# Performance work log

Hardware: AMD Instinct MI355X
Metric: run time of the kernel (lower is better)

The kernel has to match this reference:

```python
import jax, jax.numpy as jnp
import numpy as np

V, E, H, L, C, NH, O, B = 32000, 128, 128, 6, 4, 4, 1024, 16384
HD = H // NH


def setup_inputs() -> dict:
    key = jax.random.key(0)
    ks = jax.random.split(key, 20)
    s = 1.0 / np.sqrt(H).astype(np.float32)

    def rn(k, shape, scale=s):
        return jax.random.normal(k, shape, jnp.float32) * scale

    return {
        "tokens": jax.random.randint(ks[0], (B, 1), 0, V),
        "h": jax.random.normal(ks[1], (L, C, B, H), jnp.float32),
        "emb": rn(ks[2], (V, E), 1.0),
        "wih0_c0": rn(ks[3], (3 * H, E)),
        "wih0_rest": rn(ks[4], (C - 1, 3 * H, 1)),
        "bih0": rn(ks[5], (C, 3 * H)),
        "whh0": rn(ks[6], (C, 3 * H, H)),
        "bhh0": rn(ks[7], (C, 3 * H)),
        "wih": rn(ks[8], (L - 1, C, 3 * H, H)),
        "whh": rn(ks[9], (L - 1, C, 3 * H, H)),
        "bih": rn(ks[10], (L - 1, C, 3 * H)),
        "bhh": rn(ks[11], (L - 1, C, 3 * H)),
        "attn_in_w": rn(ks[12], (L, 3 * H, H)),
        "attn_in_b": rn(ks[13], (L, 3 * H)),
        "attn_out_w": rn(ks[14], (L, H, H), 0.001),  # nn.init.normal_(out_proj.weight, 0, 0.001)
        "attn_out_b": jnp.zeros((L, H), jnp.float32),
        "ln_g": jnp.ones((L, H), jnp.float32),
        "ln_b": jnp.zeros((L, H), jnp.float32),
        "gate_w": rn(ks[15], (L, 2 * H)),
        "gate_b": jnp.zeros((L,), jnp.float32),
        "head_w": rn(ks[16], (O, H)),
        "head_b": jnp.zeros((O,), jnp.float32),
    }


def _gru(gi, gh, h):
    # torch GRUCell: r,z gates sigmoid; n = tanh(in + r*hn); h' = (1-z)*n + z*h
    ir, iz, i_n = jnp.split(gi, 3, -1)
    hr, hz, h_n = jnp.split(gh, 3, -1)
    r = jax.nn.sigmoid(ir + hr)
    z = jax.nn.sigmoid(iz + hz)
    n = jnp.tanh(i_n + r * h_n)
    return (1.0 - z) * n + z * h


def _msg_layer(hn, in_w, in_b, out_w, out_b, g, b):
    # hn: [C,B,H]; MultiheadAttention with batch_first=False (seq=C), then LayerNorm
    qkv = jnp.einsum('cbh,gh->cbg', hn, in_w) + in_b
    q, k, v = jnp.split(qkv, 3, -1)
    q = q.reshape(C, -1, NH, HD)
    k = k.reshape(C, -1, NH, HD)
    v = v.reshape(C, -1, NH, HD)
    scores = jnp.einsum('qbnd,kbnd->bnqk', q, k) / np.sqrt(HD).astype(np.float32)
    a = jax.nn.softmax(scores, axis=-1)
    o = jnp.einsum('bnqk,kbnd->qbnd', a, v).reshape(C, -1, H)
    o = jnp.einsum('cbh,oh->cbo', o, out_w) + out_b
    mu = o.mean(-1, keepdims=True)
    var = o.var(-1, keepdims=True)
    return (o - mu) / jnp.sqrt(var + 1e-5) * g + b


def reference(tokens, h, emb, wih0_c0, wih0_rest, bih0, whh0, bhh0, wih, whh, bih, bhh,
              attn_in_w, attn_in_b, attn_out_w, attn_out_b, ln_g, ln_b,
              gate_w, gate_b, head_w, head_b):
    bsz = tokens.shape[0]
    x0 = emb[tokens[:, 0]]  # [B,E]
    x = None
    h_new = []
    for l in range(L):
        hl = h[l]  # [C,B,H]
        if l == 0:
            gi0 = x0 @ wih0_c0.T + bih0[0]  # col 0 gets the embedding
            # cols 1..C-1 get a zeros(B,1) dummy input -> x @ wih0_rest == 0, bias only
            gi_rest = jnp.broadcast_to(bih0[1:, None, :], (C - 1, bsz, 3 * H))
            gi = jnp.concatenate([gi0[None], gi_rest], 0)
            whh_l, bhh_l = whh0, bhh0
        else:
            gi = jnp.einsum('cbi,cgi->cbg', x, wih[l - 1]) + bih[l - 1][:, None, :]
            whh_l, bhh_l = whh[l - 1], bhh[l - 1]
        gh = jnp.einsum('cbi,cgi->cbg', hl, whh_l) + bhh_l[:, None, :]
        hl_n = _gru(gi, gh, hl)
        msg = _msg_layer(hl_n, attn_in_w[l], attn_in_b[l], attn_out_w[l], attn_out_b[l], ln_g[l], ln_b[l])
        gin = jnp.concatenate([hl_n, msg], -1)  # [C,B,2H]
        gt = jax.nn.sigmoid(jnp.einsum('cbh,h->cb', gin, gate_w[l]) + gate_b[l])[..., None]
        hl_n = (1.0 - gt) * hl_n + gt * msg
        h_new.append(hl_n)
        x = hl_n
    h_n = jnp.stack(h_new, 0)  # [L,C,B,H]
    y = h_n[-1, 0] @ head_w.T + head_b  # head on last layer, column 0
    return (y, h_n)
```

## Files before the change

kernel.cpp:

```cpp
#include <hip/hip_runtime.h>
#include <hip/hip_bf16.h>

#define B_   16384
#define H_   128
#define C_   4
#define L_   6
#define O_   1024
#define G3H  384
#define CB   (C_ * B_)
#define CBH  (C_ * B_ * H_)

typedef __hip_bfloat16 bf16;
using bf16x8  = __attribute__((ext_vector_type(8))) __bf16;
using bf16x4  = __attribute__((ext_vector_type(4))) __bf16;
using floatx4 = __attribute__((ext_vector_type(4))) float;

__device__ __forceinline__ bf16 f2bf(float x) { return __float2bfloat16(x); }
__device__ __forceinline__ float bf2f(bf16 x) { return __bfloat162float(x); }
__device__ __forceinline__ void store_val(float* p, float v) { *p = v; }
__device__ __forceinline__ void store_val(bf16* p, float v) { *p = f2bf(v); }

__device__ __forceinline__ floatx4 mfma16(bf16x8 a, bf16x8 b, floatx4 c) {
  return __builtin_amdgcn_mfma_f32_16x16x32_bf16(a, b, c, 0, 0, 0);
}

__device__ __forceinline__ bf16x8 load8(const bf16* p) { return *(const bf16x8*)p; }
__device__ __forceinline__ bf16x8 load8(const float* p) {
  const float4 a = *(const float4*)p;
  const float4 b = *(const float4*)(p + 4);
  bf16x8 r;
  r[0] = (__bf16)a.x; r[1] = (__bf16)a.y; r[2] = (__bf16)a.z; r[3] = (__bf16)a.w;
  r[4] = (__bf16)b.x; r[5] = (__bf16)b.y; r[6] = (__bf16)b.z; r[7] = (__bf16)b.w;
  return r;
}

__device__ __forceinline__ float wave_sum(float x) {
#pragma unroll
  for (int off = 32; off; off >>= 1) x += __shfl_xor(x, off);
  return x;
}

__device__ __forceinline__ float sigmoidf_(float x) {
  return 1.f / (1.f + __expf(-x));
}
__device__ __forceinline__ float tanhf_(float x) {
  float e = __expf(2.f * x);
  return 1.f - 2.f / (e + 1.f);
}

struct Cvt7 {
  const float* src[7];
  long start4[8];
};
__global__ __launch_bounds__(256) void cvt7_kernel(Cvt7 a, bf16* __restrict__ dst) {
  long i4 = (long)blockIdx.x * 256 + threadIdx.x;
  if (i4 >= a.start4[7]) return;
  int s = 0;
#pragma unroll
  for (int k = 1; k < 7; ++k)
    if (i4 >= a.start4[k]) s = k;
  const float4 v = ((const float4*)a.src[s])[i4 - a.start4[s]];
  bf16x4 o;
  o[0] = (__bf16)v.x; o[1] = (__bf16)v.y; o[2] = (__bf16)v.z; o[3] = (__bf16)v.w;
  ((bf16x4*)dst)[i4] = o;
}

template <typename AT, typename OutT>
__global__ __launch_bounds__(256) void gemm_bt(const AT* __restrict__ A,
                                               const bf16* __restrict__ W,
                                               const float* __restrict__ bias,
                                               OutT* __restrict__ out,
                                               int N, int rows_per_batch,
                                               long wstride, long bstride) {
  const int wave = threadIdx.x >> 6;
  const int lane = threadIdx.x & 63;
  const int m0   = blockIdx.x * 16;
  const int n0   = blockIdx.y * 64 + wave * 16;
  const int sub  = lane & 15;
  const int quad = lane >> 4;
  const int batch = m0 / rows_per_batch;
  const bf16*  Wb = W + (long)batch * wstride;
  const float* Bi = bias + (long)batch * bstride;

  const AT*   Ap = A + (long)(m0 + sub) * 128 + quad * 8;
  const bf16* Wp = Wb + (long)(n0 + sub) * 128 + quad * 8;

  floatx4 acc = {0.f, 0.f, 0.f, 0.f};
#pragma unroll
  for (int kc = 0; kc < 4; ++kc) {
    acc = mfma16(load8(Ap + kc * 32), load8(Wp + kc * 32), acc);
  }

  const int col = n0 + sub;
  const float bv = Bi[col];
#pragma unroll
  for (int r = 0; r < 4; ++r) {
    long row = m0 + quad * 4 + r;
    store_val(&out[row * (long)N + col], acc[r] + bv);
  }
}

__global__ __launch_bounds__(128) void embed_kernel(const int* __restrict__ tok,
                                                    const float* __restrict__ emb,
                                                    bf16* __restrict__ x0) {
  const int b = blockIdx.x;
  x0[(long)b * 128 + threadIdx.x] = f2bf(emb[(long)tok[b] * 128 + threadIdx.x]);
}

template <bool L0>
__global__ __launch_bounds__(256) void cell_fused(const float* __restrict__ x,
                                                  const bf16* __restrict__ x0,
                                                  const bf16* __restrict__ wih_l,
                                                  const float* __restrict__ bih_l,
                                                  const float* __restrict__ h,
                                                  const bf16* __restrict__ whh_l,
                                                  const float* __restrict__ bhh_l,
                                                  const bf16* __restrict__ ainw,
                                                  const float* __restrict__ ainb,
                                                  float* __restrict__ hn,
                                                  bf16* __restrict__ qkv) {
  __shared__ __align__(16) char lds[3 * 16384];
  char* h_raw  = lds;
  char* x_raw  = lds + 16384;
  char* hn_raw = lds + 32768;

  const int tid = threadIdx.x;
  const int wave = tid >> 6, lane = tid & 63;
  const int sub = lane & 15, quad = lane >> 4;
  const int m0 = blockIdx.x * 64;
  const int cell = m0 / B_;
  const bool has_gi = (!L0) || (cell == 0);

  {
    const int colg = tid & 15;
    const int rb   = tid >> 4;
#pragma unroll
    for (int i = 0; i < 4; ++i) {
      const int row = i * 16 + rb;
      bf16x8 v = load8(h + (long)(m0 + row) * H_ + colg * 8);
      const int boff = (row * 256 + colg * 16) ^ ((row & 7) << 4);
      *(bf16x8*)(h_raw + boff) = v;
    }
    if (has_gi) {
      if constexpr (L0) {
#pragma unroll
        for (int i = 0; i < 4; ++i) {
          const int row = i * 16 + rb;
          bf16x8 v = load8(x0 + (long)(m0 + row) * H_ + colg * 8);
          const int boff = (row * 256 + colg * 16) ^ ((row & 7) << 4);
          *(bf16x8*)(x_raw + boff) = v;
        }
      } else {
#pragma unroll
        for (int i = 0; i < 4; ++i) {
          const int row = i * 16 + rb;
          bf16x8 v = load8(x + (long)(m0 + row) * H_ + colg * 8);
          const int boff = (row * 256 + colg * 16) ^ ((row & 7) << 4);
          *(bf16x8*)(x_raw + boff) = v;
        }
      }
    }
  }
  __syncthreads();

  const bf16*  Wh = whh_l + (long)cell * G3H * H_;
  const bf16*  Wi = L0 ? wih_l : wih_l + (long)cell * G3H * H_;
  const float* bh = bhh_l + cell * G3H;
  const float* bi = bih_l + cell * G3H;

#pragma unroll
  for (int p = 0; p < 2; ++p) {
    const int colr = wave * 32 + p * 16 + sub;

    bf16x8 wfr[3][4], wif[3][4];
#pragma unroll
    for (int g = 0; g < 3; ++g) {
      const bf16* Wg = Wh + (long)(g * 128 + colr) * H_ + quad * 8;
#pragma unroll
      for (int kc = 0; kc < 4; ++kc) wfr[g][kc] = load8(Wg + kc * 32);
    }
    if (has_gi) {
#pragma unroll
      for (int g = 0; g < 3; ++g) {
        const bf16* Wg = Wi + (long)(g * 128 + colr) * H_ + quad * 8;
#pragma unroll
        for (int kc = 0; kc < 4; ++kc) wif[g][kc] = load8(Wg + kc * 32);
      }
    }

    const float bir = bi[colr],        bhr = bh[colr];
    const float biz = bi[128 + colr],  bhz = bh[128 + colr];
    const float bin_ = bi[256 + colr], bhn = bh[256 + colr];

#pragma unroll
    for (int rt = 0; rt < 4; ++rt) {
      bf16x8 hfr[4];
#pragma unroll
      for (int kc = 0; kc < 4; ++kc) {
        const int lrow = rt * 16 + sub;
        const int boff = (lrow * 256 + kc * 64 + quad * 16) ^ ((lrow & 7) << 4);
        hfr[kc] = *(const bf16x8*)(h_raw + boff);
      }
      floatx4 ar = {0.f, 0.f, 0.f, 0.f}, az = {0.f, 0.f, 0.f, 0.f};
      floatx4 anh = {0.f, 0.f, 0.f, 0.f}, ani = {0.f, 0.f, 0.f, 0.f};
#pragma unroll
      for (int kc = 0; kc < 4; ++kc) {
        ar  = mfma16(hfr[kc], wfr[0][kc], ar);
        az  = mfma16(hfr[kc], wfr[1][kc], az);
        anh = mfma16(hfr[kc], wfr[2][kc], anh);
      }
      if (has_gi) {
        bf16x8 xfr[4];
#pragma unroll
        for (int kc = 0; kc < 4; ++kc) {
          const int lrow = rt * 16 + sub;
          const int boff = (lrow * 256 + kc * 64 + quad * 16) ^ ((lrow & 7) << 4);
          xfr[kc] = *(const bf16x8*)(x_raw + boff);
        }
#pragma unroll
        for (int kc = 0; kc < 4; ++kc) {
          ar  = mfma16(xfr[kc], wif[0][kc], ar);
          az  = mfma16(xfr[kc], wif[1][kc], az);
          ani = mfma16(xfr[kc], wif[2][kc], ani);
        }
      }

#pragma unroll
      for (int r = 0; r < 4; ++r) {
        const int lrow = rt * 16 + quad * 4 + r;
        const long grow = m0 + lrow;
        float rg = sigmoidf_(ar[r] + bir + bhr);
        float zg = sigmoidf_(az[r] + biz + bhz);
        float ng = tanhf_(ani[r] + bin_ + rg * (anh[r] + bhn));
        float hv = h[grow * H_ + colr];
        float hnv = (1.f - zg) * ng + zg * hv;
        hn[grow * H_ + colr] = hnv;
        const int boff = (lrow * 256 + colr * 2) ^ ((lrow & 7) << 4);
        *(bf16*)(hn_raw + boff) = f2bf(hnv);
      }
    }
  }
  __syncthreads();

#pragma unroll
  for (int t = 0; t < 6; ++t) {
    const int col = wave * 96 + t * 16 + sub;
    bf16x8 wf[4];
    const bf16* Wp = ainw + (long)col * H_ + quad * 8;
#pragma unroll
    for (int kc = 0; kc < 4; ++kc) wf[kc] = load8(Wp + kc * 32);
    const float bv = ainb[col];
#pragma unroll
    for (int rp = 0; rp < 2; ++rp) {
      bf16x8 af0[4], af1[4];
#pragma unroll
      for (int kc = 0; kc < 4; ++kc) {
        const int lr0 = (2 * rp) * 16 + sub, lr1 = (2 * rp + 1) * 16 + sub;
        af0[kc] = *(const bf16x8*)(hn_raw +
                   ((lr0 * 256 + kc * 64 + quad * 16) ^ ((lr0 & 7) << 4)));
        af1[kc] = *(const bf16x8*)(hn_raw +
                   ((lr1 * 256 + kc * 64 + quad * 16) ^ ((lr1 & 7) << 4)));
      }
      floatx4 acc0 = {0.f, 0.f, 0.f, 0.f}, acc1 = {0.f, 0.f, 0.f, 0.f};
#pragma unroll
      for (int kc = 0; kc < 4; ++kc) {
        acc0 = mfma16(af0[kc], wf[kc], acc0);
        acc1 = mfma16(af1[kc], wf[kc], acc1);
      }
#pragma unroll
      for (int r = 0; r < 4; ++r) {
        qkv[(long)(m0 + (2 * rp) * 16 + quad * 4 + r) * G3H + col] = f2bf(acc0[r] + bv);
        qkv[(long)(m0 + (2 * rp + 1) * 16 + quad * 4 + r) * G3H + col] = f2bf(acc1[r] + bv);
      }
    }
  }
}

__global__ __launch_bounds__(256) void attn_oproj(const bf16* __restrict__ qkv,
                                                  const bf16* __restrict__ w,
                                                  const float* __restrict__ bias,
                                                  const float* __restrict__ g,
                                                  const float* __restrict__ bb,
                                                  const float* __restrict__ gatew,
                                                  const float* __restrict__ gateb,
                                                  float* __restrict__ hn) {
  __shared__ __align__(16) char lds[49152 + 16384];
  bf16*  qkv_s = (bf16*)lds;
  float* o2_s  = (float*)lds;
  char*  o_raw = lds + 49152;

  const int tid = threadIdx.x;
  const int b0 = blockIdx.x * 16;

#pragma unroll
  for (int i = 0; i < 12; ++i) {
    const int idx = i * 256 + tid;
    const int r = idx / 48, ch = idx - r * 48;
    const int c = r >> 4, bj = r & 15;
    bf16x8 v = load8(qkv + ((long)c * B_ + b0 + bj) * G3H + ch * 8);
    *(bf16x8*)(qkv_s + r * 384 + ch * 8) = v;
  }
  __syncthreads();

  {
    const int d = tid & 31;
    const int pair = tid >> 5;
#pragma unroll
    for (int pi = 0; pi < 8; ++pi) {
      const int idx = pi * 8 + pair;
      const int bj = idx >> 2, head = idx & 3;
      float q[C_], k[C_], v[C_];
#pragma unroll
      for (int c = 0; c < C_; ++c) {
        const bf16* row = qkv_s + (c * 16 + bj) * 384 + head * 32 + d;
        q[c] = bf2f(row[0]);
        k[c] = bf2f(row[128]);
        v[c] = bf2f(row[256]);
      }
      float a[C_][C_];
#pragma unroll
      for (int qc = 0; qc < C_; ++qc) {
#pragma unroll
        for (int kc = 0; kc < C_; ++kc) {
          float pdot = q[qc] * k[kc];
#pragma unroll
          for (int off = 16; off; off >>= 1) pdot += __shfl_xor(pdot, off, 32);
          a[qc][kc] = pdot * 0.17677669529663687f;
        }
      }
#pragma unroll
      for (int qc = 0; qc < C_; ++qc) {
        float m = fmaxf(fmaxf(a[qc][0], a[qc][1]), fmaxf(a[qc][2], a[qc][3]));
        float s = 0.f;
#pragma unroll
        for (int kc = 0; kc < C_; ++kc) {
          a[qc][kc] = __expf(a[qc][kc] - m);
          s += a[qc][kc];
        }
        float inv = 1.f / s;
        float ov = 0.f;
#pragma unroll
        for (int kc = 0; kc < C_; ++kc) ov += a[qc][kc] * v[kc];
        const int orow = qc * 16 + bj;
        const int boff = (orow * 256 + (head * 32 + d) * 2) ^ ((orow & 7) << 4);
        *(bf16*)(o_raw + boff) = f2bf(ov * inv);
      }
    }
  }
  __syncthreads();

  {
    const int wave = tid >> 6, lane = tid & 63;
    const int sub = lane & 15, quad = lane >> 4;
#pragma unroll
    for (int p = 0; p < 2; ++p) {
      const int col = wave * 32 + p * 16 + sub;
      bf16x8 wf[4];
      const bf16* Wp = w + (long)col * H_ + quad * 8;
#pragma unroll
      for (int kc = 0; kc < 4; ++kc) wf[kc] = load8(Wp + kc * 32);
      const float bv = bias[col];
#pragma unroll
      for (int rt = 0; rt < 4; ++rt) {
        bf16x8 af[4];
#pragma unroll
        for (int kc = 0; kc < 4; ++kc) {
          const int lrow = rt * 16 + sub;
          af[kc] = *(const bf16x8*)(o_raw +
                    ((lrow * 256 + kc * 64 + quad * 16) ^ ((lrow & 7) << 4)));
        }
        floatx4 acc = {0.f, 0.f, 0.f, 0.f};
#pragma unroll
        for (int kc = 0; kc < 4; ++kc) acc = mfma16(af[kc], wf[kc], acc);
#pragma unroll
        for (int r = 0; r < 4; ++r)
          o2_s[(rt * 16 + quad * 4 + r) * 132 + col] = acc[r] + bv;
      }
    }
  }
  __syncthreads();

  {
    const int wave = tid >> 6, lane = tid & 63;
#pragma unroll
    for (int rr = 0; rr < 16; ++rr) {
      const int row = wave * 16 + rr;
      const int j1 = lane, j2 = lane + 64;
      float v1 = o2_s[row * 132 + j1], v2 = o2_s[row * 132 + j2];
      float mu = wave_sum(v1 + v2) * (1.f / 128.f);
      float d1 = v1 - mu, d2 = v2 - mu;
      float var = wave_sum(d1 * d1 + d2 * d2) * (1.f / 128.f);
      float rs = rsqrtf(var + 1e-5f);
      float m1 = d1 * rs * g[j1] + bb[j1];
      float m2 = d2 * rs * g[j2] + bb[j2];
      const int qc = row >> 4, bj = row & 15;
      const long grow = (long)qc * B_ + b0 + bj;
      float h1 = hn[grow * H_ + j1], h2 = hn[grow * H_ + j2];
      float gp = h1 * gatew[j1] + m1 * gatew[128 + j1] +
                 h2 * gatew[j2] + m2 * gatew[128 + j2];
      float gt = 1.f / (1.f + __expf(-(wave_sum(gp) + gateb[0])));
      hn[grow * H_ + j1] = (1.f - gt) * h1 + gt * m1;
      hn[grow * H_ + j2] = (1.f - gt) * h2 + gt * m2;
    }
  }
}

extern "C" void kernel_launch(void* const* d_in, const int* in_sizes, int n_in,
                              void* d_out, int out_size, void* d_ws, size_t ws_size,
                              hipStream_t stream) {
  const int*   tokens = (const int*)d_in[0];
  const float* h      = (const float*)d_in[1];
  const float* emb    = (const float*)d_in[2];
  const float* wih0c0 = (const float*)d_in[3];
  const float* bih0   = (const float*)d_in[5];
  const float* whh0   = (const float*)d_in[6];
  const float* bhh0   = (const float*)d_in[7];
  const float* wih    = (const float*)d_in[8];
  const float* whh    = (const float*)d_in[9];
  const float* bih    = (const float*)d_in[10];
  const float* bhh    = (const float*)d_in[11];
  const float* ainw   = (const float*)d_in[12];
  const float* ainb   = (const float*)d_in[13];
  const float* aoutw  = (const float*)d_in[14];
  const float* aoutb  = (const float*)d_in[15];
  const float* lng    = (const float*)d_in[16];
  const float* lnb    = (const float*)d_in[17];
  const float* gw     = (const float*)d_in[18];
  const float* gb     = (const float*)d_in[19];
  const float* headw  = (const float*)d_in[20];
  const float* headb  = (const float*)d_in[21];

  float* y_out  = (float*)d_out;
  float* hn_out = (float*)d_out + (long)B_ * O_;

  bf16* ws = (bf16*)d_ws;
  bf16* bufA = ws;
  bf16* x0   = bufA + (long)CB * G3H;
  bf16* wp   = x0 + (long)CB * H_;
  bf16* wih0bf  = wp;                  wp += 49152;
  bf16* whh0bf  = wp;                  wp += 196608;
  bf16* wihbf   = wp;                  wp += 983040;
  bf16* whhbf   = wp;                  wp += 983040;
  bf16* ainwbf  = wp;                  wp += 294912;
  bf16* aoutwbf = wp;                  wp += 98304;
  bf16* headwbf = wp;                  wp += 131072;

  dim3 blk(256);

  {
    Cvt7 a;
    const float* srcs[7] = {wih0c0, whh0, wih, whh, ainw, aoutw, headw};
    const long lens[7] = {49152, 196608, 983040, 983040, 294912, 98304, 131072};
    long cum = 0;
    for (int i = 0; i < 7; ++i) { a.src[i] = srcs[i]; a.start4[i] = cum / 4; cum += lens[i]; }
    a.start4[7] = cum / 4;
    const long n4 = cum / 4;
    cvt7_kernel<<<(int)((n4 + 255) / 256), blk, 0, stream>>>(a, wih0bf);
  }

  embed_kernel<<<B_, 128, 0, stream>>>(tokens, emb, x0);

  for (int l = 0; l < L_; ++l) {
    float* hn_l = hn_out + (long)l * CBH;
    const float* hl = h + (long)l * CBH;

    if (l == 0) {
      cell_fused<true><<<CB / 64, blk, 0, stream>>>(
          nullptr, x0, wih0bf, bih0, hl, whh0bf, bhh0,
          ainwbf, ainb, hn_l, bufA);
    } else {
      cell_fused<false><<<CB / 64, blk, 0, stream>>>(
          hn_out + (long)(l - 1) * CBH, nullptr,
          wihbf + (long)(l - 1) * C_ * G3H * H_, bih + (long)(l - 1) * C_ * G3H,
          hl, whhbf + (long)(l - 1) * C_ * G3H * H_, bhh + (long)(l - 1) * C_ * G3H,
          ainwbf + (long)l * G3H * H_, ainb + (long)l * G3H, hn_l, bufA);
    }

    attn_oproj<<<B_ / 16, blk, 0, stream>>>(
        bufA, aoutwbf + (long)l * H_ * H_, aoutb + (long)l * H_,
        lng + l * H_, lnb + l * H_, gw + l * 2 * H_, gb + l, hn_l);
  }

  gemm_bt<float, float><<<dim3(B_ / 16, O_ / 64), blk, 0, stream>>>(
      hn_out + (long)5 * CBH, headwbf, headb, y_out, O_, B_, 0, 0);
}
```

Baseline: 1.288 ms.

## Fuse embedding gather, stage QKV in LDS, MFMA attention, retile head GEMM

Removes the separate embedding kernel by gathering embedding rows directly inside the layer-0 cell kernel. The cell kernel now stages QKV output in LDS and writes it out with coalesced vector stores, and preloads hn fragments once. The attention kernel computes scores with MFMA and a shuffle-based softmax, applies V with vectorized LDS reads, and caches LN and gate parameters in LDS. The layernorm and gate step is vectorized with four threads per row. The head GEMM is replaced by a 64x256 tiled kernel that reuses A fragments across columns. Together these touch many unrelated parts of the pipeline and raise LDS use in the attention kernel, which could reduce occupancy.

Result: faster. 1.074 ms (-16.6%).

```diff
diff --git a/kernel.cpp b/kernel.cpp
--- a/kernel.cpp
+++ b/kernel.cpp
@@ -17,8 +17,6 @@
 
 __device__ __forceinline__ bf16 f2bf(float x) { return __float2bfloat16(x); }
 __device__ __forceinline__ float bf2f(bf16 x) { return __bfloat162float(x); }
-__device__ __forceinline__ void store_val(float* p, float v) { *p = v; }
-__device__ __forceinline__ void store_val(bf16* p, float v) { *p = f2bf(v); }
 
 __device__ __forceinline__ floatx4 mfma16(bf16x8 a, bf16x8 b, floatx4 c) {
   return __builtin_amdgcn_mfma_f32_16x16x32_bf16(a, b, c, 0, 0, 0);
@@ -34,12 +32,6 @@
   return r;
 }
 
-__device__ __forceinline__ float wave_sum(float x) {
-#pragma unroll
-  for (int off = 32; off; off >>= 1) x += __shfl_xor(x, off);
-  return x;
-}
-
 __device__ __forceinline__ float sigmoidf_(float x) {
   return 1.f / (1.f + __expf(-x));
 }
@@ -65,51 +57,10 @@
   ((bf16x4*)dst)[i4] = o;
 }
 
-template <typename AT, typename OutT>
-__global__ __launch_bounds__(256) void gemm_bt(const AT* __restrict__ A,
-                                               const bf16* __restrict__ W,
-                                               const float* __restrict__ bias,
-                                               OutT* __restrict__ out,
-                                               int N, int rows_per_batch,
-                                               long wstride, long bstride) {
-  const int wave = threadIdx.x >> 6;
-  const int lane = threadIdx.x & 63;
-  const int m0   = blockIdx.x * 16;
-  const int n0   = blockIdx.y * 64 + wave * 16;
-  const int sub  = lane & 15;
-  const int quad = lane >> 4;
-  const int batch = m0 / rows_per_batch;
-  const bf16*  Wb = W + (long)batch * wstride;
-  const float* Bi = bias + (long)batch * bstride;
-
-  const AT*   Ap = A + (long)(m0 + sub) * 128 + quad * 8;
-  const bf16* Wp = Wb + (long)(n0 + sub) * 128 + quad * 8;
-
-  floatx4 acc = {0.f, 0.f, 0.f, 0.f};
-#pragma unroll
-  for (int kc = 0; kc < 4; ++kc) {
-    acc = mfma16(load8(Ap + kc * 32), load8(Wp + kc * 32), acc);
-  }
-
-  const int col = n0 + sub;
-  const float bv = Bi[col];
-#pragma unroll
-  for (int r = 0; r < 4; ++r) {
-    long row = m0 + quad * 4 + r;
-    store_val(&out[row * (long)N + col], acc[r] + bv);
-  }
-}
-
-__global__ __launch_bounds__(128) void embed_kernel(const int* __restrict__ tok,
-                                                    const float* __restrict__ emb,
-                                                    bf16* __restrict__ x0) {
-  const int b = blockIdx.x;
-  x0[(long)b * 128 + threadIdx.x] = f2bf(emb[(long)tok[b] * 128 + threadIdx.x]);
-}
-
 template <bool L0>
 __global__ __launch_bounds__(256) void cell_fused(const float* __restrict__ x,
-                                                  const bf16* __restrict__ x0,
+                                                  const int* __restrict__ tok,
+                                                  const float* __restrict__ emb,
                                                   const bf16* __restrict__ wih_l,
                                                   const float* __restrict__ bih_l,
                                                   const float* __restrict__ h,
@@ -123,6 +74,7 @@
   char* h_raw  = lds;
   char* x_raw  = lds + 16384;
   char* hn_raw = lds + 32768;
+  char* qkv_raw = lds;
 
   const int tid = threadIdx.x;
   const int wave = tid >> 6, lane = tid & 63;
@@ -138,25 +90,23 @@
     for (int i = 0; i < 4; ++i) {
       const int row = i * 16 + rb;
       bf16x8 v = load8(h + (long)(m0 + row) * H_ + colg * 8);
-      const int boff = (row * 256 + colg * 16) ^ ((row & 7) << 4);
-      *(bf16x8*)(h_raw + boff) = v;
+      *(bf16x8*)(h_raw + ((row * 256 + colg * 16) ^ ((row & 7) << 4))) = v;
     }
     if (has_gi) {
       if constexpr (L0) {
 #pragma unroll
         for (int i = 0; i < 4; ++i) {
           const int row = i * 16 + rb;
-          bf16x8 v = load8(x0 + (long)(m0 + row) * H_ + colg * 8);
-          const int boff = (row * 256 + colg * 16) ^ ((row & 7) << 4);
-          *(bf16x8*)(x_raw + boff) = v;
+          const int tk = tok[m0 + row];
+          bf16x8 v = load8(emb + (long)tk * 128 + colg * 8);
+          *(bf16x8*)(x_raw + ((row * 256 + colg * 16) ^ ((row & 7) << 4))) = v;
         }
       } else {
 #pragma unroll
         for (int i = 0; i < 4; ++i) {
           const int row = i * 16 + rb;
           bf16x8 v = load8(x + (long)(m0 + row) * H_ + colg * 8);
-          const int boff = (row * 256 + colg * 16) ^ ((row & 7) << 4);
-          *(bf16x8*)(x_raw + boff) = v;
+          *(bf16x8*)(x_raw + ((row * 256 + colg * 16) ^ ((row & 7) << 4))) = v;
         }
       }
     }
@@ -198,8 +148,8 @@
 #pragma unroll
       for (int kc = 0; kc < 4; ++kc) {
         const int lrow = rt * 16 + sub;
-        const int boff = (lrow * 256 + kc * 64 + quad * 16) ^ ((lrow & 7) << 4);
-        hfr[kc] = *(const bf16x8*)(h_raw + boff);
+        hfr[kc] = *(const bf16x8*)(h_raw +
+                   ((lrow * 256 + kc * 64 + quad * 16) ^ ((lrow & 7) << 4)));
       }
       floatx4 ar = {0.f, 0.f, 0.f, 0.f}, az = {0.f, 0.f, 0.f, 0.f};
       floatx4 anh = {0.f, 0.f, 0.f, 0.f}, ani = {0.f, 0.f, 0.f, 0.f};
@@ -214,8 +164,8 @@
 #pragma unroll
         for (int kc = 0; kc < 4; ++kc) {
           const int lrow = rt * 16 + sub;
-          const int boff = (lrow * 256 + kc * 64 + quad * 16) ^ ((lrow & 7) << 4);
-          xfr[kc] = *(const bf16x8*)(x_raw + boff);
+          xfr[kc] = *(const bf16x8*)(x_raw +
+                     ((lrow * 256 + kc * 64 + quad * 16) ^ ((lrow & 7) << 4)));
         }
 #pragma unroll
         for (int kc = 0; kc < 4; ++kc) {
@@ -235,9 +185,20 @@
         float hv = h[grow * H_ + colr];
         float hnv = (1.f - zg) * ng + zg * hv;
         hn[grow * H_ + colr] = hnv;
-        const int boff = (lrow * 256 + colr * 2) ^ ((lrow & 7) << 4);
-        *(bf16*)(hn_raw + boff) = f2bf(hnv);
-      }
+        *(bf16*)(hn_raw + ((lrow * 256 + colr * 2) ^ ((lrow & 7) << 4))) = f2bf(hnv);
+      }
+    }
+  }
+  __syncthreads();
+
+  bf16x8 af[4][4];
+#pragma unroll
+  for (int rt = 0; rt < 4; ++rt) {
+#pragma unroll
+    for (int kc = 0; kc < 4; ++kc) {
+      const int lrow = rt * 16 + sub;
+      af[rt][kc] = *(const bf16x8*)(hn_raw +
+                    ((lrow * 256 + kc * 64 + quad * 16) ^ ((lrow & 7) << 4)));
     }
   }
   __syncthreads();
@@ -251,28 +212,26 @@
     for (int kc = 0; kc < 4; ++kc) wf[kc] = load8(Wp + kc * 32);
     const float bv = ainb[col];
 #pragma unroll
-    for (int rp = 0; rp < 2; ++rp) {
-      bf16x8 af0[4], af1[4];
-#pragma unroll
-      for (int kc = 0; kc < 4; ++kc) {
-        const int lr0 = (2 * rp) * 16 + sub, lr1 = (2 * rp + 1) * 16 + sub;
-        af0[kc] = *(const bf16x8*)(hn_raw +
-                   ((lr0 * 256 + kc * 64 + quad * 16) ^ ((lr0 & 7) << 4)));
-        af1[kc] = *(const bf16x8*)(hn_raw +
-                   ((lr1 * 256 + kc * 64 + quad * 16) ^ ((lr1 & 7) << 4)));
-      }
-      floatx4 acc0 = {0.f, 0.f, 0.f, 0.f}, acc1 = {0.f, 0.f, 0.f, 0.f};
-#pragma unroll
-      for (int kc = 0; kc < 4; ++kc) {
-        acc0 = mfma16(af0[kc], wf[kc], acc0);
-        acc1 = mfma16(af1[kc], wf[kc], acc1);
-      }
+    for (int rt = 0; rt < 4; ++rt) {
+      floatx4 acc = {0.f, 0.f, 0.f, 0.f};
+#pragma unroll
+      for (int kc = 0; kc < 4; ++kc) acc = mfma16(af[rt][kc], wf[kc], acc);
 #pragma unroll
       for (int r = 0; r < 4; ++r) {
-        qkv[(long)(m0 + (2 * rp) * 16 + quad * 4 + r) * G3H + col] = f2bf(acc0[r] + bv);
-        qkv[(long)(m0 + (2 * rp + 1) * 16 + quad * 4 + r) * G3H + col] = f2bf(acc1[r] + bv);
-      }
-    }
+        const int lrow = rt * 16 + quad * 4 + r;
+        *(bf16*)(qkv_raw + ((lrow * 768 + col * 2) ^ ((lrow & 12) << 3))) =
+            f2bf(acc[r] + bv);
+      }
+    }
+  }
+  __syncthreads();
+
+#pragma unroll
+  for (int i = 0; i < 12; ++i) {
+    const int m = i * 256 + tid;
+    const int row = m / 48, ch = m - row * 48;
+    bf16x8 v = *(const bf16x8*)(qkv_raw + ((row * 768 + ch * 16) ^ ((row & 12) << 3)));
+    *(bf16x8*)(qkv + (long)(m0 + row) * G3H + ch * 8) = v;
   }
 }
 
@@ -284,12 +243,16 @@
                                                   const float* __restrict__ gatew,
                                                   const float* __restrict__ gateb,
                                                   float* __restrict__ hn) {
-  __shared__ __align__(16) char lds[49152 + 16384];
-  bf16*  qkv_s = (bf16*)lds;
+  __shared__ __align__(16) char lds[50176 + 4096 + 16384 + 2048];
+  char*  qbase = lds;
+  float* p_s   = (float*)(lds + 50176);
+  char*  o_raw = lds + 50176 + 4096;
+  float* prm   = (float*)(lds + 50176 + 4096 + 16384);
   float* o2_s  = (float*)lds;
-  char*  o_raw = lds + 49152;
 
   const int tid = threadIdx.x;
+  const int wave = tid >> 6, lane = tid & 63;
+  const int sub = lane & 15, quad = lane >> 4;
   const int b0 = blockIdx.x * 16;
 
 #pragma unroll
@@ -298,60 +261,84 @@
     const int r = idx / 48, ch = idx - r * 48;
     const int c = r >> 4, bj = r & 15;
     bf16x8 v = load8(qkv + ((long)c * B_ + b0 + bj) * G3H + ch * 8);
-    *(bf16x8*)(qkv_s + r * 384 + ch * 8) = v;
+    *(bf16x8*)(qbase + r * 784 + ch * 16) = v;
+  }
+  if (tid < 128) {
+    prm[tid] = g[tid];
+    prm[128 + tid] = bb[tid];
+    prm[256 + tid] = gatew[tid];
+    prm[384 + tid] = gatew[128 + tid];
   }
   __syncthreads();
 
   {
-    const int d = tid & 31;
-    const int pair = tid >> 5;
-#pragma unroll
-    for (int pi = 0; pi < 8; ++pi) {
-      const int idx = pi * 8 + pair;
-      const int bj = idx >> 2, head = idx & 3;
-      float q[C_], k[C_], v[C_];
-#pragma unroll
-      for (int c = 0; c < C_; ++c) {
-        const bf16* row = qkv_s + (c * 16 + bj) * 384 + head * 32 + d;
-        q[c] = bf2f(row[0]);
-        k[c] = bf2f(row[128]);
-        v[c] = bf2f(row[256]);
-      }
-      float a[C_][C_];
-#pragma unroll
-      for (int qc = 0; qc < C_; ++qc) {
-#pragma unroll
-        for (int kc = 0; kc < C_; ++kc) {
-          float pdot = q[qc] * k[kc];
-#pragma unroll
-          for (int off = 16; off; off >>= 1) pdot += __shfl_xor(pdot, off, 32);
-          a[qc][kc] = pdot * 0.17677669529663687f;
-        }
-      }
-#pragma unroll
-      for (int qc = 0; qc < C_; ++qc) {
-        float m = fmaxf(fmaxf(a[qc][0], a[qc][1]), fmaxf(a[qc][2], a[qc][3]));
-        float s = 0.f;
-#pragma unroll
-        for (int kc = 0; kc < C_; ++kc) {
-          a[qc][kc] = __expf(a[qc][kc] - m);
-          s += a[qc][kc];
-        }
-        float inv = 1.f / s;
-        float ov = 0.f;
-#pragma unroll
-        for (int kc = 0; kc < C_; ++kc) ov += a[qc][kc] * v[kc];
-        const int orow = qc * 16 + bj;
-        const int boff = (orow * 256 + (head * 32 + d) * 2) ^ ((orow & 7) << 4);
-        *(bf16*)(o_raw + boff) = f2bf(ov * inv);
-      }
-    }
+    const int hd = wave;
+    const int bi = sub >> 2, qc = sub & 3;
+    const int bjx = sub >> 2, kc = sub & 3;
+#pragma unroll
+    for (int bg = 0; bg < 4; ++bg) {
+      const int rq = qc * 16 + bg * 4 + bi;
+      const int rk = kc * 16 + bg * 4 + bjx;
+      bf16x8 qa = *(const bf16x8*)(qbase + rq * 784 + hd * 64 + quad * 16);
+      bf16x8 kb = *(const bf16x8*)(qbase + rk * 784 + 256 + hd * 64 + quad * 16);
+      floatx4 sc = {0.f, 0.f, 0.f, 0.f};
+      sc = mfma16(qa, kb, sc);
+      float p[4];
+#pragma unroll
+      for (int r = 0; r < 4; ++r) {
+        float s = sc[r] * 0.17677669529663687f;
+        float m = fmaxf(s, __shfl_xor(s, 1));
+        m = fmaxf(m, __shfl_xor(m, 2));
+        float e = __expf(s - m);
+        float ssum = e + __shfl_xor(e, 1);
+        ssum += __shfl_xor(ssum, 2);
+        p[r] = e / ssum;
+      }
+      if (quad == bjx) {
+        const int bl = bg * 4 + quad;
+#pragma unroll
+        for (int r = 0; r < 4; ++r)
+          p_s[((bl * 4 + hd) * 4 + r) * 4 + kc] = p[r];
+      }
+    }
+  }
+  __syncthreads();
+
+#pragma unroll
+  for (int i = 0; i < 4; ++i) {
+    const int m = i * 256 + tid;
+    const int row = m >> 4;
+    const int ch = m & 15;
+    const int qc = row >> 4, bj = row & 15;
+    const int hd = ch >> 2;
+    float acc[8];
+#pragma unroll
+    for (int j = 0; j < 8; ++j) acc[j] = 0.f;
+#pragma unroll
+    for (int kc = 0; kc < 4; ++kc) {
+      const float pv = p_s[((bj * 4 + hd) * 4 + qc) * 4 + kc];
+      bf16x8 vv = *(const bf16x8*)(qbase + (kc * 16 + bj) * 784 + 512 + ch * 16);
+#pragma unroll
+      for (int j = 0; j < 8; ++j) acc[j] += pv * (float)vv[j];
+    }
+    bf16x8 ov;
+#pragma unroll
+    for (int j = 0; j < 8; ++j) ov[j] = (__bf16)acc[j];
+    *(bf16x8*)(o_raw + ((row * 256 + ch * 16) ^ ((row & 7) << 4))) = ov;
   }
   __syncthreads();
 
   {
-    const int wave = tid >> 6, lane = tid & 63;
-    const int sub = lane & 15, quad = lane >> 4;
+    bf16x8 af[4][4];
+#pragma unroll
+    for (int rt = 0; rt < 4; ++rt) {
+#pragma unroll
+      for (int kc = 0; kc < 4; ++kc) {
+        const int lrow = rt * 16 + sub;
+        af[rt][kc] = *(const bf16x8*)(o_raw +
+                      ((lrow * 256 + kc * 64 + quad * 16) ^ ((lrow & 7) << 4)));
+      }
+    }
 #pragma unroll
     for (int p = 0; p < 2; ++p) {
       const int col = wave * 32 + p * 16 + sub;
@@ -362,16 +349,9 @@
       const float bv = bias[col];
 #pragma unroll
       for (int rt = 0; rt < 4; ++rt) {
-        bf16x8 af[4];
-#pragma unroll
-        for (int kc = 0; kc < 4; ++kc) {
-          const int lrow = rt * 16 + sub;
-          af[kc] = *(const bf16x8*)(o_raw +
-                    ((lrow * 256 + kc * 64 + quad * 16) ^ ((lrow & 7) << 4)));
-        }
         floatx4 acc = {0.f, 0.f, 0.f, 0.f};
 #pragma unroll
-        for (int kc = 0; kc < 4; ++kc) acc = mfma16(af[kc], wf[kc], acc);
+        for (int kc = 0; kc < 4; ++kc) acc = mfma16(af[rt][kc], wf[kc], acc);
 #pragma unroll
         for (int r = 0; r < 4; ++r)
           o2_s[(rt * 16 + quad * 4 + r) * 132 + col] = acc[r] + bv;
@@ -381,26 +361,111 @@
   __syncthreads();
 
   {
-    const int wave = tid >> 6, lane = tid & 63;
-#pragma unroll
-    for (int rr = 0; rr < 16; ++rr) {
-      const int row = wave * 16 + rr;
-      const int j1 = lane, j2 = lane + 64;
-      float v1 = o2_s[row * 132 + j1], v2 = o2_s[row * 132 + j2];
-      float mu = wave_sum(v1 + v2) * (1.f / 128.f);
-      float d1 = v1 - mu, d2 = v2 - mu;
-      float var = wave_sum(d1 * d1 + d2 * d2) * (1.f / 128.f);
-      float rs = rsqrtf(var + 1e-5f);
-      float m1 = d1 * rs * g[j1] + bb[j1];
-      float m2 = d2 * rs * g[j2] + bb[j2];
-      const int qc = row >> 4, bj = row & 15;
-      const long grow = (long)qc * B_ + b0 + bj;
-      float h1 = hn[grow * H_ + j1], h2 = hn[grow * H_ + j2];
-      float gp = h1 * gatew[j1] + m1 * gatew[128 + j1] +
-                 h2 * gatew[j2] + m2 * gatew[128 + j2];
-      float gt = 1.f / (1.f + __expf(-(wave_sum(gp) + gateb[0])));
-      hn[grow * H_ + j1] = (1.f - gt) * h1 + gt * m1;
-      hn[grow * H_ + j2] = (1.f - gt) * h2 + gt * m2;
+    const int row = tid >> 2;
+    const int c0 = (tid & 3) * 32;
+    float s = 0.f;
+#pragma unroll
+    for (int j = 0; j < 32; j += 4) {
+      float4 v = *(const float4*)&o2_s[row * 132 + c0 + j];
+      s += v.x + v.y + v.z + v.w;
+    }
+    s += __shfl_xor(s, 1);
+    s += __shfl_xor(s, 2);
+    const float mu = s * (1.f / 128.f);
+    float vs = 0.f;
+#pragma unroll
+    for (int j = 0; j < 32; j += 4) {
+      float4 v = *(const float4*)&o2_s[row * 132 + c0 + j];
+      float d0 = v.x - mu, d1 = v.y - mu, d2 = v.z - mu, d3 = v.w - mu;
+      vs += d0 * d0 + d1 * d1 + d2 * d2 + d3 * d3;
+    }
+    vs += __shfl_xor(vs, 1);
+    vs += __shfl_xor(vs, 2);
+    const float rs = rsqrtf(vs * (1.f / 128.f) + 1e-5f);
+
+    const int qc = row >> 4, bj = row & 15;
+    const long grow = (long)qc * B_ + b0 + bj;
+    float mv[32], hv[32];
+    float gp = 0.f;
+#pragma unroll
+    for (int j = 0; j < 32; j += 4) {
+      float4 v = *(const float4*)&o2_s[row * 132 + c0 + j];
+      float4 hh = *(const float4*)&hn[grow * H_ + c0 + j];
+      float vv[4] = {v.x, v.y, v.z, v.w};
+      float hh4[4] = {hh.x, hh.y, hh.z, hh.w};
+#pragma unroll
+      for (int q = 0; q < 4; ++q) {
+        const int c = c0 + j + q;
+        float mval = (vv[q] - mu) * rs * prm[c] + prm[128 + c];
+        mv[j + q] = mval;
+        hv[j + q] = hh4[q];
+        gp += hh4[q] * prm[256 + c] + mval * prm[384 + c];
+      }
+    }
+    gp += __shfl_xor(gp, 1);
+    gp += __shfl_xor(gp, 2);
+    const float gt = 1.f / (1.f + __expf(-(gp + gateb[0])));
+#pragma unroll
+    for (int j = 0; j < 32; j += 4) {
+      float4 o;
+      o.x = (1.f - gt) * hv[j]     + gt * mv[j];
+      o.y = (1.f - gt) * hv[j + 1] + gt * mv[j + 1];
+      o.z = (1.f - gt) * hv[j + 2] + gt * mv[j + 2];
+      o.w = (1.f - gt) * hv[j + 3] + gt * mv[j + 3];
+      *(float4*)&hn[grow * H_ + c0 + j] = o;
+    }
+  }
+}
+
+__global__ __launch_bounds__(256) void head_gemm(const float* __restrict__ A,
+                                                 const bf16* __restrict__ W,
+                                                 const float* __restrict__ bias,
+                                                 float* __restrict__ out) {
+  __shared__ __align__(16) char a_raw[64 * 256];
+  const int tid = threadIdx.x;
+  const int wave = tid >> 6, lane = tid & 63;
+  const int sub = lane & 15, quad = lane >> 4;
+  const int m0 = blockIdx.x * 64;
+  const int nb = blockIdx.y * 256;
+
+  {
+    const int colg = tid & 15;
+    const int rb = tid >> 4;
+#pragma unroll
+    for (int i = 0; i < 4; ++i) {
+      const int row = i * 16 + rb;
+      bf16x8 v = load8(A + (long)(m0 + row) * H_ + colg * 8);
+      *(bf16x8*)(a_raw + ((row * 256 + colg * 16) ^ ((row & 7) << 4))) = v;
+    }
+  }
+  __syncthreads();
+
+  bf16x8 af[4][4];
+#pragma unroll
+  for (int rt = 0; rt < 4; ++rt) {
+#pragma unroll
+    for (int kc = 0; kc < 4; ++kc) {
+      const int lrow = rt * 16 + sub;
+      af[rt][kc] = *(const bf16x8*)(a_raw +
+                    ((lrow * 256 + kc * 64 + quad * 16) ^ ((lrow & 7) << 4)));
+    }
+  }
+#pragma unroll
+  for (int ct = 0; ct < 4; ++ct) {
+    const int col = nb + wave * 64 + ct * 16 + sub;
+    bf16x8 wf[4];
+    const bf16* Wp = W + (long)col * H_ + quad * 8;
+#pragma unroll
+    for (int kc = 0; kc < 4; ++kc) wf[kc] = load8(Wp + kc * 32);
+    const float bv = bias[col];
+#pragma unroll
+    for (int rt = 0; rt < 4; ++rt) {
+      floatx4 acc = {0.f, 0.f, 0.f, 0.f};
+#pragma unroll
+      for (int kc = 0; kc < 4; ++kc) acc = mfma16(af[rt][kc], wf[kc], acc);
+#pragma unroll
+      for (int r = 0; r < 4; ++r)
+        out[(long)(m0 + rt * 16 + quad * 4 + r) * O_ + col] = acc[r] + bv;
     }
   }
 }
@@ -435,8 +500,7 @@
 
   bf16* ws = (bf16*)d_ws;
   bf16* bufA = ws;
-  bf16* x0   = bufA + (long)CB * G3H;
-  bf16* wp   = x0 + (long)CB * H_;
+  bf16* wp   = bufA + (long)CB * G3H;
   bf16* wih0bf  = wp;                  wp += 49152;
   bf16* whh0bf  = wp;                  wp += 196608;
   bf16* wihbf   = wp;                  wp += 983040;
@@ -458,19 +522,17 @@
     cvt7_kernel<<<(int)((n4 + 255) / 256), blk, 0, stream>>>(a, wih0bf);
   }
 
-  embed_kernel<<<B_, 128, 0, stream>>>(tokens, emb, x0);
-
   for (int l = 0; l < L_; ++l) {
     float* hn_l = hn_out + (long)l * CBH;
     const float* hl = h + (long)l * CBH;
 
     if (l == 0) {
       cell_fused<true><<<CB / 64, blk, 0, stream>>>(
-          nullptr, x0, wih0bf, bih0, hl, whh0bf, bhh0,
+          nullptr, tokens, emb, wih0bf, bih0, hl, whh0bf, bhh0,
           ainwbf, ainb, hn_l, bufA);
     } else {
       cell_fused<false><<<CB / 64, blk, 0, stream>>>(
-          hn_out + (long)(l - 1) * CBH, nullptr,
+          hn_out + (long)(l - 1) * CBH, nullptr, nullptr,
           wihbf + (long)(l - 1) * C_ * G3H * H_, bih + (long)(l - 1) * C_ * G3H,
           hl, whhbf + (long)(l - 1) * C_ * G3H * H_, bhh + (long)(l - 1) * C_ * G3H,
           ainwbf + (long)l * G3H * H_, ainb + (long)l * G3H, hn_l, bufA);
@@ -481,6 +543,6 @@
         lng + l * H_, lnb + l * H_, gw + l * 2 * H_, gb + l, hn_l);
   }
 
-  gemm_bt<float, float><<<dim3(B_ / 16, O_ / 64), blk, 0, stream>>>(
-      hn_out + (long)5 * CBH, headwbf, headb, y_out, O_, B_, 0, 0);
-}
+  head_gemm<<<dim3(B_ / 64, O_ / 256), blk, 0, stream>>>(
+      hn_out + (long)5 * CBH, headwbf, headb, y_out);
+}
```
